# Performance work log

Hardware: AMD Instinct MI355X
Metric: run time of the kernel (lower is better)

## Reference

```python
import jax, jax.numpy as jnp
import numpy as np

B, T = 512, 64
A, H, R = 6, 256, 256
SS, SD = 32, 32          # stochastic_size, stochastic_dim
L = SS * SD              # latent_dim = 1024


def setup_inputs() -> dict:
    key = jax.random.key(0)
    ks = jax.random.split(key, 12)
    s = 0.05
    obs = jax.random.normal(ks[0], (B, T, H), dtype=jnp.float32)
    action = jax.random.normal(ks[1], (B, T, A), dtype=jnp.float32)
    first = jax.random.bernoulli(ks[2], 0.1, (B, T, 1))
    u = jax.random.uniform(ks[3], (T, B, SS, SD), minval=1e-6, maxval=1.0 - 1e-6)
    gumbel = -jnp.log(-jnp.log(u))  # Gumbel(0,1) noise for categorical sampling
    W_in = jax.random.normal(ks[4], (H, L + A)) * s
    b_in = jax.random.normal(ks[5], (H,)) * s
    W_ih = jax.random.normal(ks[6], (3 * R, H)) * s
    W_hh = jax.random.normal(ks[7], (3 * R, R)) * s
    b_ih = jax.random.normal(ks[8], (3 * R,)) * s
    b_hh = jax.random.normal(ks[9], (3 * R,)) * s
    W_post = jax.random.normal(ks[10], (L, R + H)) * s
    b_post = jax.random.normal(ks[11], (L,)) * s
    return {"obs": obs, "action": action, "first": first, "gumbel": gumbel,
            "W_in": W_in, "b_in": b_in, "W_ih": W_ih, "W_hh": W_hh,
            "b_ih": b_ih, "b_hh": b_hh, "W_post": W_post, "b_post": b_post}


def reference(obs, action, first, gumbel, W_in, b_in, W_ih, W_hh, b_ih, b_hh, W_post, b_post):
    bs = obs.shape[0]
    rec = W_hh.shape[1]
    latent = W_post.shape[0]
    size, dim = gumbel.shape[-2], gumbel.shape[-1]

    def step(carry, xs):
        deter, stoch = carry
        o, a, f, g = xs  # per-timestep slices
        # reset to initial (zeros) where episode starts
        deter = jnp.where(f, 0.0, deter)
        stoch = jnp.where(f, 0.0, stoch)
        # img_step: in-linear + GRUCell (torch gate order r, z, n)
        x = jnp.concatenate([stoch, a], axis=-1) @ W_in.T + b_in
        gi = x @ W_ih.T + b_ih
        gh = deter @ W_hh.T + b_hh
        i_r, i_z, i_n = jnp.split(gi, 3, axis=-1)
        h_r, h_z, h_n = jnp.split(gh, 3, axis=-1)
        r = jax.nn.sigmoid(i_r + h_r)
        z = jax.nn.sigmoid(i_z + h_z)
        n = jnp.tanh(i_n + r * h_n)
        h = (1.0 - z) * n + z * deter  # new deter
        # posterior head + categorical sample (Gumbel-max, non-differentiable)
        logits = jnp.concatenate([h, o], axis=-1) @ W_post.T + b_post
        lg = logits.reshape(bs, size, dim)
        idx = jnp.argmax(lg + g, axis=-1)
        stoch_new = jax.nn.one_hot(idx, dim, dtype=logits.dtype).reshape(bs, latent)
        return (h, stoch_new), (h, stoch_new, logits)

    carry0 = (jnp.zeros((bs, rec), obs.dtype), jnp.zeros((bs, latent), obs.dtype))
    xs = (jnp.swapaxes(obs, 0, 1), jnp.swapaxes(action, 0, 1),
          jnp.swapaxes(first, 0, 1), gumbel)
    _, (deter_seq, stoch_seq, logits_seq) = jax.lax.scan(step, carry0, xs)
    # back to batch-first [B, T, ...]
    return (jnp.swapaxes(deter_seq, 0, 1),
            jnp.swapaxes(stoch_seq, 0, 1),
            jnp.swapaxes(logits_seq, 0, 1))
```

## Files before the change

### kernel.cpp

```cpp
#include <hip/hip_runtime.h>
#include <math.h>

#define BB   512
#define TT   64
#define AD   6
#define HD   256
#define RD   256
#define LD   1024
#define GD   768
#define NB   2

#define OFF_WIHT    0u
#define OFF_WHHT    196608u
#define OFF_WPOSTT  393216u
#define OFF_WCT     917504u
#define OFF_BC      1708544u
#define OFF_OBSPROJ 1709312u
#define WS_FLOATS_FULL (OFF_OBSPROJ + (size_t)32768 * 1024)

__device__ __forceinline__ void fma4(float4& a, const float4 w, const float s) {
  a.x = fmaf(w.x, s, a.x); a.y = fmaf(w.y, s, a.y);
  a.z = fmaf(w.z, s, a.z); a.w = fmaf(w.w, s, a.w);
}
__device__ __forceinline__ void fma2(float2& a, const float2 w, const float s) {
  a.x = fmaf(w.x, s, a.x); a.y = fmaf(w.y, s, a.y);
}
typedef float fvec4 __attribute__((ext_vector_type(4)));
__device__ __forceinline__ float4 ntload4(const float* p) {
  const fvec4 v = __builtin_nontemporal_load((const fvec4*)p);
  return make_float4(v.x, v.y, v.z, v.w);
}
__device__ __forceinline__ void ntstore4(float* p, const float4 v) {
  fvec4 w; w.x = v.x; w.y = v.y; w.z = v.z; w.w = v.w;
  __builtin_nontemporal_store(w, (fvec4*)p);
}

__global__ __launch_bounds__(256) void transpose_k(const float* __restrict__ src,
                                                   float* __restrict__ dst,
                                                   int R, int C) {
  __shared__ float t_s[32][33];
  const int tx = threadIdx.x, ty = threadIdx.y;
  const int c0 = blockIdx.x * 32, r0 = blockIdx.y * 32;
#pragma unroll
  for (int k = 0; k < 4; ++k)
    t_s[ty + k*8][tx] = src[(size_t)(r0 + ty + k*8) * C + c0 + tx];
  __syncthreads();
#pragma unroll
  for (int k = 0; k < 4; ++k)
    dst[(size_t)(c0 + ty + k*8) * R + r0 + tx] = t_s[tx][ty + k*8];
}

__global__ __launch_bounds__(256) void wc_kernel(const float* __restrict__ W_in,
                                                 const float* __restrict__ b_in,
                                                 const float* __restrict__ WihT,
                                                 const float* __restrict__ b_ih,
                                                 float* __restrict__ WcT,
                                                 float* __restrict__ bc) {
  __shared__ float v_s[256];
  const int tid = threadIdx.x;
  const int col = blockIdx.x;
  v_s[tid] = (col < 1030) ? W_in[(size_t)tid * 1030 + col] : b_in[tid];
  __syncthreads();
  float a0 = 0.f, a1 = 0.f, a2 = 0.f;
#pragma unroll 4
  for (int h = 0; h < 256; ++h) {
    const float v = v_s[h];
    const float* row = &WihT[(size_t)h * GD];
    a0 = fmaf(row[tid      ], v, a0);
    a1 = fmaf(row[tid + 256], v, a1);
    a2 = fmaf(row[tid + 512], v, a2);
  }
  if (col < 1030) {
    WcT[(size_t)col * GD + tid      ] = a0;
    WcT[(size_t)col * GD + tid + 256] = a1;
    WcT[(size_t)col * GD + tid + 512] = a2;
  } else {
    bc[tid      ] = b_ih[tid      ] + a0;
    bc[tid + 256] = b_ih[tid + 256] + a1;
    bc[tid + 512] = b_ih[tid + 512] + a2;
  }
}

__global__ __launch_bounds__(256) void obsproj_gemm(const float* __restrict__ obs,
                                                    const float* __restrict__ Wpost,
                                                    const float* __restrict__ bpost,
                                                    float* __restrict__ outp) {
  __shared__ __align__(16) float As[32][132];
  __shared__ __align__(16) float Bs[32][132];
  const int tid = threadIdx.x;
  const int tx = tid & 15, ty = tid >> 4;
  const int m0 = blockIdx.y * 128, n0 = blockIdx.x * 128;
  float acc[8][8];
#pragma unroll
  for (int i = 0; i < 8; ++i)
#pragma unroll
    for (int j = 0; j < 8; ++j) acc[i][j] = 0.f;

  for (int k0 = 0; k0 < 256; k0 += 32) {
#pragma unroll
    for (int it = 0; it < 4; ++it) {
      const int idx = tid + it * 256;
      const int mi = idx >> 3, k4 = (idx & 7) * 4;
      float4 va = *(const float4*)&obs[(size_t)(m0 + mi) * 256 + k0 + k4];
      As[k4+0][mi] = va.x; As[k4+1][mi] = va.y; As[k4+2][mi] = va.z; As[k4+3][mi] = va.w;
      float4 vb = *(const float4*)&Wpost[(size_t)(n0 + mi) * 512 + 256 + k0 + k4];
      Bs[k4+0][mi] = vb.x; Bs[k4+1][mi] = vb.y; Bs[k4+2][mi] = vb.z; Bs[k4+3][mi] = vb.w;
    }
    __syncthreads();
#pragma unroll 8
    for (int k = 0; k < 32; ++k) {
      float4 a0 = *(const float4*)&As[k][ty*4];
      float4 a1 = *(const float4*)&As[k][64 + ty*4];
      float4 b0 = *(const float4*)&Bs[k][tx*4];
      float4 b1 = *(const float4*)&Bs[k][64 + tx*4];
      float av[8] = {a0.x,a0.y,a0.z,a0.w,a1.x,a1.y,a1.z,a1.w};
      float bv[8] = {b0.x,b0.y,b0.z,b0.w,b1.x,b1.y,b1.z,b1.w};
#pragma unroll
      for (int i = 0; i < 8; ++i)
#pragma unroll
        for (int j = 0; j < 8; ++j) acc[i][j] = fmaf(av[i], bv[j], acc[i][j]);
    }
    __syncthreads();
  }
  float4 bp0 = *(const float4*)&bpost[n0 + tx*4];
  float4 bp1 = *(const float4*)&bpost[n0 + 64 + tx*4];
#pragma unroll
  for (int i = 0; i < 8; ++i) {
    const int mi = (i < 4) ? (ty*4 + i) : (64 + ty*4 + (i - 4));
    float4 c0, c1;
    c0.x = acc[i][0] + bp0.x; c0.y = acc[i][1] + bp0.y;
    c0.z = acc[i][2] + bp0.z; c0.w = acc[i][3] + bp0.w;
    c1.x = acc[i][4] + bp1.x; c1.y = acc[i][5] + bp1.y;
    c1.z = acc[i][6] + bp1.z; c1.w = acc[i][7] + bp1.w;
    ntstore4(&outp[(size_t)(m0 + mi) * 1024 + n0 + tx*4], c0);
    ntstore4(&outp[(size_t)(m0 + mi) * 1024 + n0 + 64 + tx*4], c1);
  }
}

#define GH_LOAD(W, g) {                                                   \
    const int cg_ = (g) * 4;                                              \
    W[0] = wp[(size_t)(cg_ + 0) * 192];                                   \
    W[1] = wp[(size_t)(cg_ + 1) * 192];                                   \
    W[2] = wp[(size_t)(cg_ + 2) * 192];                                   \
    W[3] = wp[(size_t)(cg_ + 3) * 192];                                   \
  }
#define GH_LOADL(W) {                                                     \
    W[0] = ((const float4*)wpin_gh[half][0])[rg];                         \
    W[1] = ((const float4*)wpin_gh[half][1])[rg];                         \
    W[2] = ((const float4*)wpin_gh[half][2])[rg];                         \
    W[3] = ((const float4*)wpin_gh[half][3])[rg];                         \
  }
#define GH_FMA(W, g) {                                                    \
    const int cg_ = (g) * 4;                                              \
    const float4 d0 = *(const float4*)&deter_s[0][cbase + cg_];           \
    const float4 d1 = *(const float4*)&deter_s[1][cbase + cg_];           \
    fma4(acc0, W[0], d0.x); fma4(acc0, W[1], d0.y); fma4(acc0, W[2], d0.z); fma4(acc0, W[3], d0.w); \
    fma4(acc1, W[0], d1.x); fma4(acc1, W[1], d1.y); fma4(acc1, W[2], d1.z); fma4(acc1, W[3], d1.w); \
  }
#define GI_LOAD(W, g) {                                                   \
    W[0] = ntload4((const float*)&Wc4[(size_t)scol_s[j][(g)*4 + 0] * 192 + rg]); \
    W[1] = ntload4((const float*)&Wc4[(size_t)scol_s[j][(g)*4 + 1] * 192 + rg]); \
    W[2] = ntload4((const float*)&Wc4[(size_t)scol_s[j][(g)*4 + 2] * 192 + rg]); \
    W[3] = ntload4((const float*)&Wc4[(size_t)scol_s[j][(g)*4 + 3] * 192 + rg]); \
  }
#define GI_ADD(W) {                                                       \
    acc.x += W[0].x; acc.y += W[0].y; acc.z += W[0].z; acc.w += W[0].w;   \
    acc.x += W[1].x; acc.y += W[1].y; acc.z += W[1].z; acc.w += W[1].w;   \
    acc.x += W[2].x; acc.y += W[2].y; acc.z += W[2].z; acc.w += W[2].w;   \
    acc.x += W[3].x; acc.y += W[3].y; acc.z += W[3].z; acc.w += W[3].w;   \
  }
#define PP_LOAD(W, g) {                                                   \
    const int cg_ = (g) * 4;                                              \
    W[0] = pp2w[(size_t)(cg_ + 0) * 512];                                 \
    W[1] = pp2w[(size_t)(cg_ + 1) * 512];                                 \
    W[2] = pp2w[(size_t)(cg_ + 2) * 512];                                 \
    W[3] = pp2w[(size_t)(cg_ + 3) * 512];                                 \
  }
#define PP_LOADL(W, g) {                                                  \
    W[0] = ((const float2*)wpin_pp[half][g][0])[o2];                      \
    W[1] = ((const float2*)wpin_pp[half][g][1])[o2];                      \
    W[2] = ((const float2*)wpin_pp[half][g][2])[o2];                      \
    W[3] = ((const float2*)wpin_pp[half][g][3])[o2];                      \
  }
#define PP_FMA(W, g) {                                                    \
    const int cg_ = (g) * 4;                                              \
    const float4 d0 = *(const float4*)&deter_s[0][cbase + cg_];           \
    const float4 d1 = *(const float4*)&deter_s[1][cbase + cg_];           \
    fma2(acc0, W[0], d0.x); fma2(acc0, W[1], d0.y); fma2(acc0, W[2], d0.z); fma2(acc0, W[3], d0.w); \
    fma2(acc1, W[0], d1.x); fma2(acc1, W[1], d1.y); fma2(acc1, W[2], d1.z); fma2(acc1, W[3], d1.w); \
  }

__global__ __launch_bounds__(1024, 4) void rssm_scan(
    const float* __restrict__ obs, const float* __restrict__ action,
    const int* __restrict__ first, const float* __restrict__ gumbel,
    const float* __restrict__ WhhT, const float* __restrict__ WpostT,
    const float* __restrict__ WcT, const float* __restrict__ bc,
    const float* __restrict__ bhh, const float* __restrict__ bpost,
    const float* __restrict__ obsproj,
    float* __restrict__ out_deter, float* __restrict__ out_stoch,
    float* __restrict__ out_logits) {
  union SharedU {
    struct { float gi[NB][GD]; float ghp[2][NB][GD]; } g;
    float pp[2][NB][LD];
  };
  __shared__ SharedU u;
  __shared__ __align__(16) float deter_s[NB][RD];
  __shared__ __align__(16) float obs_s[NB][HD];
  __shared__ float act_all[NB][TT][AD];
  __shared__ int   first_all[NB][TT];
  __shared__ float bc_s[GD];
  __shared__ float bhh_s[GD];
  __shared__ int   scol_s[NB][32];
  __shared__ __align__(16) float wpin_gh[2][4][768];
  __shared__ __align__(16) float wpin_pp[2][2][4][1024];

  const int tid = threadIdx.x;
  const int b0 = blockIdx.x * NB;
  const bool use_op = (obsproj != nullptr);
  const float4* Wc4 = (const float4*)WcT;
  const float4* Wh4 = (const float4*)WhhT;
  const float2* Wp2 = (const float2*)WpostT;

  if (tid < NB * RD) deter_s[tid >> 8][tid & 255] = 0.f;
  if (tid < NB * TT * AD) {
    const int j = tid / (TT * AD), rem = tid % (TT * AD);
    act_all[j][rem / AD][rem % AD] = action[(size_t)(b0 + j) * TT * AD + rem];
  }
  if (tid < NB * TT) first_all[tid >> 6][tid & 63] = first[(b0 + (tid >> 6)) * TT + (tid & 63)];
  if (tid < GD) { bc_s[tid] = bc[tid]; bhh_s[tid] = bhh[tid]; }
  for (int i = tid; i < 1536; i += 1024) {
    const int hf = i / 768, r = i % 768, c = r / 192, rg = r % 192;
    ((float4*)wpin_gh[hf][c])[rg] = Wh4[(size_t)(hf * 128 + c) * 192 + rg];
  }
  for (int i = tid; i < 4096; i += 1024) {
    const int hf = i / 2048, r = i % 2048, g = r / 1024, r2 = r % 1024;
    const int c = r2 / 256, q = r2 % 256;
    ((float4*)wpin_pp[hf][g][c])[q] =
        ((const float4*)(WpostT + (size_t)(hf * 128 + g * 4 + c) * 1024))[q];
  }
  __syncthreads();

  const int jme = tid >> 8, o4me = tid & 255;

  for (int t = 0; t < TT; ++t) {
    float4 op4, g4;
    if (tid < NB * 256) {
      if (use_op)
        op4 = ntload4(&obsproj[(((size_t)(b0 + jme) * TT + t) * LD) + o4me * 4]);
      else
        op4 = *(const float4*)&bpost[o4me * 4];
      g4 = ntload4(&gumbel[(((size_t)t * BB + b0 + jme) * LD) + o4me * 4]);
    }

    if (tid < 384) {
      const int half = (tid < 192) ? 0 : 1;
      const int rg = tid - half * 192;
      const int cbase = half * 128;
      float4 acc0, acc1;
      if (half == 0) {
        acc0 = *(const float4*)&bhh_s[rg * 4];
        acc1 = acc0;
      } else {
        acc0 = make_float4(0.f, 0.f, 0.f, 0.f);
        acc1 = acc0;
      }
      const float4* wp = &Wh4[(size_t)cbase * 192 + rg];
      float4 wA[4], wB[4], wC[4];
      GH_LOAD(wA, 1); GH_LOAD(wB, 2);
      GH_LOADL(wC); GH_FMA(wC, 0);
#pragma unroll 1
      for (int gg = 0; gg < 9; ++gg) {
        const int g = 1 + gg * 3;
        GH_LOAD(wC, g + 2); GH_FMA(wA, g);
        GH_LOAD(wA, g + 3); GH_FMA(wB, g + 1);
        GH_LOAD(wB, g + 4); GH_FMA(wC, g + 2);
      }
      GH_LOAD(wC, 30); GH_FMA(wA, 28);
      GH_LOAD(wA, 31); GH_FMA(wB, 29);
      GH_FMA(wC, 30); GH_FMA(wA, 31);
      *(float4*)&u.g.ghp[half][0][rg * 4] = acc0;
      *(float4*)&u.g.ghp[half][1][rg * 4] = acc1;
    } else if (tid < 768) {
      const int task = tid - 384;
      const int j = task / 192, rg = task % 192;
      float4 acc = *(const float4*)&bc_s[rg * 4];
#pragma unroll
      for (int a = 0; a < AD; ++a)
        fma4(acc, Wc4[(size_t)(LD + a) * 192 + rg], act_all[j][t][a]);
      const bool skip = (t == 0) || first_all[j][t];
      if (!skip) {
        float4 gA[4], gB[4], gC[4];
        GI_LOAD(gA, 0); GI_LOAD(gB, 1);
#pragma unroll 1
        for (int gg = 0; gg < 2; ++gg) {
          const int g = gg * 3;
          GI_LOAD(gC, g + 2); GI_ADD(gA);
          GI_LOAD(gA, g + 3); GI_ADD(gB);
          GI_LOAD(gB, g + 4); GI_ADD(gC);
        }
        GI_ADD(gA); GI_ADD(gB);
      }
      *(float4*)&u.g.gi[j][rg * 4] = acc;
    } else {
      if (!use_op) {
        const int z = tid - 768;
        if (z < NB * 64) {
          const int j = z >> 6, r4 = z & 63;
          *(float4*)&obs_s[j][r4 * 4] =
              ntload4(&obs[((size_t)(b0 + j) * TT + t) * HD + r4 * 4]);
        }
      }
    }
    __syncthreads();

    if (tid < NB * RD) {
      const int j = tid >> 8, r = tid & 255;
      const float ir = u.g.gi[j][r], iz = u.g.gi[j][r + 256], inn = u.g.gi[j][r + 512];
      const float hr = u.g.ghp[0][j][r      ] + u.g.ghp[1][j][r      ];
      const float hz = u.g.ghp[0][j][r + 256] + u.g.ghp[1][j][r + 256];
      const float hn = u.g.ghp[0][j][r + 512] + u.g.ghp[1][j][r + 512];
      const bool f = (first_all[j][t] != 0);
      const float dprev = f ? 0.f : deter_s[j][r];
      const float rr = 1.f / (1.f + __expf(-(ir + hr)));
      const float zz = 1.f / (1.f + __expf(-(iz + hz)));
      const float nn = tanhf(fmaf(rr, hn, inn));
      const float h = (1.f - zz) * nn + zz * dprev;
      deter_s[j][r] = h;
      __builtin_nontemporal_store(h, &out_deter[((size_t)(b0 + j) * TT + t) * RD + r]);
    }
    __syncthreads();

    {
      const int half = tid >> 9, o2 = tid & 511;
      const int cbase = half * 128;
      float2 acc0 = make_float2(0.f, 0.f), acc1 = acc0;
      const float2* pp2w = &Wp2[(size_t)cbase * 512 + o2];
      float2 pA[4], pB[4], pC[4];
      PP_LOAD(pA, 2); PP_LOAD(pB, 3);
      PP_LOADL(pC, 0); PP_FMA(pC, 0);
      PP_LOADL(pC, 1); PP_FMA(pC, 1);
#pragma unroll 1
      for (int gg = 0; gg < 9; ++gg) {
        const int g = 2 + gg * 3;
        PP_LOAD(pC, g + 2); PP_FMA(pA, g);
        PP_LOAD(pA, g + 3); PP_FMA(pB, g + 1);
        PP_LOAD(pB, g + 4); PP_FMA(pC, g + 2);
      }
      PP_LOAD(pC, 31); PP_FMA(pA, 29);
      PP_FMA(pB, 30); PP_FMA(pC, 31);
      if (!use_op) {
#pragma unroll 4
        for (int c = 0; c < 128; c += 4) {
          const float2 w0 = Wp2[(size_t)(256 + cbase + c + 0) * 512 + o2];
          const float2 w1 = Wp2[(size_t)(256 + cbase + c + 1) * 512 + o2];
          const float2 w2 = Wp2[(size_t)(256 + cbase + c + 2) * 512 + o2];
          const float2 w3 = Wp2[(size_t)(256 + cbase + c + 3) * 512 + o2];
          const float4 o0 = *(const float4*)&obs_s[0][cbase + c];
          const float4 o1 = *(const float4*)&obs_s[1][cbase + c];
          fma2(acc0, w0, o0.x); fma2(acc0, w1, o0.y); fma2(acc0, w2, o0.z); fma2(acc0, w3, o0.w);
          fma2(acc1, w0, o1.x); fma2(acc1, w1, o1.y); fma2(acc1, w2, o1.z); fma2(acc1, w3, o1.w);
        }
      }
      *(float2*)&u.pp[half][0][o2 * 2] = acc0;
      *(float2*)&u.pp[half][1][o2 * 2] = acc1;
    }
    __syncthreads();

    {
      if (tid < NB * 256) {
        const float4 p0 = *(const float4*)&u.pp[0][jme][o4me * 4];
        const float4 p1 = *(const float4*)&u.pp[1][jme][o4me * 4];
        float4 l;
        l.x = p0.x + p1.x + op4.x; l.y = p0.y + p1.y + op4.y;
        l.z = p0.z + p1.z + op4.z; l.w = p0.w + p1.w + op4.w;
        ntstore4(&out_logits[((size_t)(b0 + jme) * TT + t) * LD + o4me * 4], l);
        float v[4] = {l.x + g4.x, l.y + g4.y, l.z + g4.z, l.w + g4.w};
        const int l0 = o4me * 4;
        float mv = v[0]; int mi = l0;
#pragma unroll
        for (int i = 1; i < 4; ++i)
          if (v[i] > mv) { mv = v[i]; mi = l0 + i; }
#pragma unroll
        for (int off = 1; off < 8; off <<= 1) {
          const float ov = __shfl_xor(mv, off);
          const int   oi = __shfl_xor(mi, off);
          if (ov > mv || (ov == mv && oi < mi)) { mv = ov; mi = oi; }
        }
        if ((o4me & 7) == 0) scol_s[jme][o4me >> 3] = mi;
        float4 oh;
        oh.x = (mi == l0 + 0) ? 1.f : 0.f;
        oh.y = (mi == l0 + 1) ? 1.f : 0.f;
        oh.z = (mi == l0 + 2) ? 1.f : 0.f;
        oh.w = (mi == l0 + 3) ? 1.f : 0.f;
        ntstore4(&out_stoch[((size_t)(b0 + jme) * TT + t) * LD + l0], oh);
      }
      if (tid < NB * 64) {
        const int j2 = tid >> 6, r4 = tid & 63;
        if (t + 1 < TT && first_all[j2][t + 1])
          *(float4*)&deter_s[j2][r4 * 4] = make_float4(0.f, 0.f, 0.f, 0.f);
      }
    }
    __syncthreads();
  }
}

extern "C" void kernel_launch(void* const* d_in, const int* in_sizes, int n_in,
                              void* d_out, int out_size, void* d_ws, size_t ws_size,
                              hipStream_t stream) {
  const float* obs    = (const float*)d_in[0];
  const float* action = (const float*)d_in[1];
  const int*   first  = (const int*)d_in[2];
  const float* gumbel = (const float*)d_in[3];
  const float* W_in   = (const float*)d_in[4];
  const float* b_in   = (const float*)d_in[5];
  const float* W_ih   = (const float*)d_in[6];
  const float* W_hh   = (const float*)d_in[7];
  const float* b_ih   = (const float*)d_in[8];
  const float* b_hh   = (const float*)d_in[9];
  const float* W_post = (const float*)d_in[10];
  const float* b_post = (const float*)d_in[11];

  float* ws      = (float*)d_ws;
  float* WihT    = ws + OFF_WIHT;
  float* WhhT    = ws + OFF_WHHT;
  float* WpostT  = ws + OFF_WPOSTT;
  float* WcT     = ws + OFF_WCT;
  float* bc      = ws + OFF_BC;
  float* obsproj = ws + OFF_OBSPROJ;
  const bool use_op = ws_size >= WS_FLOATS_FULL * sizeof(float);

  float* out_deter  = (float*)d_out;
  float* out_stoch  = out_deter + (size_t)BB * TT * RD;
  float* out_logits = out_stoch + (size_t)BB * TT * LD;

  transpose_k<<<dim3(256/32, 768/32), dim3(32, 8), 0, stream>>>(W_ih, WihT, 768, 256);
  transpose_k<<<dim3(256/32, 768/32), dim3(32, 8), 0, stream>>>(W_hh, WhhT, 768, 256);
  transpose_k<<<dim3(512/32, 1024/32), dim3(32, 8), 0, stream>>>(W_post, WpostT, 1024, 512);
  wc_kernel<<<1031, 256, 0, stream>>>(W_in, b_in, WihT, b_ih, WcT, bc);
  if (use_op)
    obsproj_gemm<<<dim3(1024/128, 32768/128), 256, 0, stream>>>(obs, W_post, b_post, obsproj);
  rssm_scan<<<BB/NB, 1024, 0, stream>>>(obs, action, first, gumbel, WhhT, WpostT, WcT, bc,
                                        b_hh, b_post, use_op ? obsproj : (const float*)nullptr,
                                        out_deter, out_stoch, out_logits);
}
```

Before: 2.597 ms.

## Process one batch row per block instead of two, doubling grid size

Each block of the recurrent scan now handles a single sequence instead of two, so the grid grows from 256 to 512 blocks and the launch-bounds occupancy hint is raised. The shared-memory pinned copy of the first W_post rows is removed, the projection loop restarts from row zero, and Wc gather loads lose their nontemporal hint. The aim is more parallel blocks and less shared memory per block, which may let more blocks fit on each CU. The cost is that each weight load from global memory now feeds only one sequence, which roughly doubles total weight traffic.

```diff
diff --git a/kernel.cpp b/kernel.cpp
--- a/kernel.cpp
+++ b/kernel.cpp
@@ -8,7 +8,6 @@
 #define RD   256
 #define LD   1024
 #define GD   768
-#define NB   2
 
 #define OFF_WIHT    0u
 #define OFF_WHHT    196608u
@@ -152,16 +151,14 @@
   }
 #define GH_FMA(W, g) {                                                    \
     const int cg_ = (g) * 4;                                              \
-    const float4 d0 = *(const float4*)&deter_s[0][cbase + cg_];           \
-    const float4 d1 = *(const float4*)&deter_s[1][cbase + cg_];           \
+    const float4 d0 = *(const float4*)&deter_s[cbase + cg_];              \
     fma4(acc0, W[0], d0.x); fma4(acc0, W[1], d0.y); fma4(acc0, W[2], d0.z); fma4(acc0, W[3], d0.w); \
-    fma4(acc1, W[0], d1.x); fma4(acc1, W[1], d1.y); fma4(acc1, W[2], d1.z); fma4(acc1, W[3], d1.w); \
   }
 #define GI_LOAD(W, g) {                                                   \
-    W[0] = ntload4((const float*)&Wc4[(size_t)scol_s[j][(g)*4 + 0] * 192 + rg]); \
-    W[1] = ntload4((const float*)&Wc4[(size_t)scol_s[j][(g)*4 + 1] * 192 + rg]); \
-    W[2] = ntload4((const float*)&Wc4[(size_t)scol_s[j][(g)*4 + 2] * 192 + rg]); \
-    W[3] = ntload4((const float*)&Wc4[(size_t)scol_s[j][(g)*4 + 3] * 192 + rg]); \
+    W[0] = Wc4[(size_t)scol_s[(g)*4 + 0] * 192 + rg];                     \
+    W[1] = Wc4[(size_t)scol_s[(g)*4 + 1] * 192 + rg];                     \
+    W[2] = Wc4[(size_t)scol_s[(g)*4 + 2] * 192 + rg];                     \
+    W[3] = Wc4[(size_t)scol_s[(g)*4 + 3] * 192 + rg];                     \
   }
 #define GI_ADD(W) {                                                       \
     acc.x += W[0].x; acc.y += W[0].y; acc.z += W[0].z; acc.w += W[0].w;   \
@@ -176,21 +173,13 @@
     W[2] = pp2w[(size_t)(cg_ + 2) * 512];                                 \
     W[3] = pp2w[(size_t)(cg_ + 3) * 512];                                 \
   }
-#define PP_LOADL(W, g) {                                                  \
-    W[0] = ((const float2*)wpin_pp[half][g][0])[o2];                      \
-    W[1] = ((const float2*)wpin_pp[half][g][1])[o2];                      \
-    W[2] = ((const float2*)wpin_pp[half][g][2])[o2];                      \
-    W[3] = ((const float2*)wpin_pp[half][g][3])[o2];                      \
-  }
 #define PP_FMA(W, g) {                                                    \
     const int cg_ = (g) * 4;                                              \
-    const float4 d0 = *(const float4*)&deter_s[0][cbase + cg_];           \
-    const float4 d1 = *(const float4*)&deter_s[1][cbase + cg_];           \
+    const float4 d0 = *(const float4*)&deter_s[cbase + cg_];              \
     fma2(acc0, W[0], d0.x); fma2(acc0, W[1], d0.y); fma2(acc0, W[2], d0.z); fma2(acc0, W[3], d0.w); \
-    fma2(acc1, W[0], d1.x); fma2(acc1, W[1], d1.y); fma2(acc1, W[2], d1.z); fma2(acc1, W[3], d1.w); \
-  }
-
-__global__ __launch_bounds__(1024, 4) void rssm_scan(
+  }
+
+__global__ __launch_bounds__(1024, 8) void rssm_scan(
     const float* __restrict__ obs, const float* __restrict__ action,
     const int* __restrict__ first, const float* __restrict__ gumbel,
     const float* __restrict__ WhhT, const float* __restrict__ WpostT,
@@ -200,70 +189,55 @@
     float* __restrict__ out_deter, float* __restrict__ out_stoch,
     float* __restrict__ out_logits) {
   union SharedU {
-    struct { float gi[NB][GD]; float ghp[2][NB][GD]; } g;
-    float pp[2][NB][LD];
+    struct { float gi[GD]; float ghp[2][GD]; } g;
+    float pp[2][LD];
   };
   __shared__ SharedU u;
-  __shared__ __align__(16) float deter_s[NB][RD];
-  __shared__ __align__(16) float obs_s[NB][HD];
-  __shared__ float act_all[NB][TT][AD];
-  __shared__ int   first_all[NB][TT];
+  __shared__ __align__(16) float deter_s[RD];
+  __shared__ __align__(16) float obs_s[HD];
+  __shared__ float act_all[TT][AD];
+  __shared__ int   first_all[TT];
   __shared__ float bc_s[GD];
   __shared__ float bhh_s[GD];
-  __shared__ int   scol_s[NB][32];
+  __shared__ int   scol_s[32];
   __shared__ __align__(16) float wpin_gh[2][4][768];
-  __shared__ __align__(16) float wpin_pp[2][2][4][1024];
 
   const int tid = threadIdx.x;
-  const int b0 = blockIdx.x * NB;
+  const int b0 = blockIdx.x;
   const bool use_op = (obsproj != nullptr);
   const float4* Wc4 = (const float4*)WcT;
   const float4* Wh4 = (const float4*)WhhT;
   const float2* Wp2 = (const float2*)WpostT;
 
-  if (tid < NB * RD) deter_s[tid >> 8][tid & 255] = 0.f;
-  if (tid < NB * TT * AD) {
-    const int j = tid / (TT * AD), rem = tid % (TT * AD);
-    act_all[j][rem / AD][rem % AD] = action[(size_t)(b0 + j) * TT * AD + rem];
-  }
-  if (tid < NB * TT) first_all[tid >> 6][tid & 63] = first[(b0 + (tid >> 6)) * TT + (tid & 63)];
+  if (tid < RD) deter_s[tid] = 0.f;
+  if (tid < TT * AD) act_all[tid / AD][tid % AD] = action[(size_t)b0 * TT * AD + tid];
+  if (tid < TT) first_all[tid] = first[b0 * TT + tid];
   if (tid < GD) { bc_s[tid] = bc[tid]; bhh_s[tid] = bhh[tid]; }
   for (int i = tid; i < 1536; i += 1024) {
     const int hf = i / 768, r = i % 768, c = r / 192, rg = r % 192;
     ((float4*)wpin_gh[hf][c])[rg] = Wh4[(size_t)(hf * 128 + c) * 192 + rg];
   }
-  for (int i = tid; i < 4096; i += 1024) {
-    const int hf = i / 2048, r = i % 2048, g = r / 1024, r2 = r % 1024;
-    const int c = r2 / 256, q = r2 % 256;
-    ((float4*)wpin_pp[hf][g][c])[q] =
-        ((const float4*)(WpostT + (size_t)(hf * 128 + g * 4 + c) * 1024))[q];
-  }
   __syncthreads();
 
-  const int jme = tid >> 8, o4me = tid & 255;
+  const int o4me = tid & 255;
 
   for (int t = 0; t < TT; ++t) {
     float4 op4, g4;
-    if (tid < NB * 256) {
+    if (tid < 256) {
       if (use_op)
-        op4 = ntload4(&obsproj[(((size_t)(b0 + jme) * TT + t) * LD) + o4me * 4]);
+        op4 = ntload4(&obsproj[(((size_t)b0 * TT + t) * LD) + o4me * 4]);
       else
         op4 = *(const float4*)&bpost[o4me * 4];
-      g4 = ntload4(&gumbel[(((size_t)t * BB + b0 + jme) * LD) + o4me * 4]);
+      g4 = ntload4(&gumbel[(((size_t)t * BB + b0) * LD) + o4me * 4]);
     }
 
     if (tid < 384) {
       const int half = (tid < 192) ? 0 : 1;
       const int rg = tid - half * 192;
       const int cbase = half * 128;
-      float4 acc0, acc1;
-      if (half == 0) {
-        acc0 = *(const float4*)&bhh_s[rg * 4];
-        acc1 = acc0;
-      } else {
-        acc0 = make_float4(0.f, 0.f, 0.f, 0.f);
-        acc1 = acc0;
-      }
+      float4 acc0;
+      if (half == 0) acc0 = *(const float4*)&bhh_s[rg * 4];
+      else           acc0 = make_float4(0.f, 0.f, 0.f, 0.f);
       const float4* wp = &Wh4[(size_t)cbase * 192 + rg];
       float4 wA[4], wB[4], wC[4];
       GH_LOAD(wA, 1); GH_LOAD(wB, 2);
@@ -278,16 +252,14 @@
       GH_LOAD(wC, 30); GH_FMA(wA, 28);
       GH_LOAD(wA, 31); GH_FMA(wB, 29);
       GH_FMA(wC, 30); GH_FMA(wA, 31);
-      *(float4*)&u.g.ghp[half][0][rg * 4] = acc0;
-      *(float4*)&u.g.ghp[half][1][rg * 4] = acc1;
-    } else if (tid < 768) {
-      const int task = tid - 384;
-      const int j = task / 192, rg = task % 192;
+      *(float4*)&u.g.ghp[half][rg * 4] = acc0;
+    } else if (tid < 576) {
+      const int rg = tid - 384;
       float4 acc = *(const float4*)&bc_s[rg * 4];
 #pragma unroll
       for (int a = 0; a < AD; ++a)
-        fma4(acc, Wc4[(size_t)(LD + a) * 192 + rg], act_all[j][t][a]);
-      const bool skip = (t == 0) || first_all[j][t];
+        fma4(acc, Wc4[(size_t)(LD + a) * 192 + rg], act_all[t][a]);
+      const bool skip = (t == 0) || first_all[t];
       if (!skip) {
         float4 gA[4], gB[4], gC[4];
         GI_LOAD(gA, 0); GI_LOAD(gB, 1);
@@ -300,54 +272,50 @@
         }
         GI_ADD(gA); GI_ADD(gB);
       }
-      *(float4*)&u.g.gi[j][rg * 4] = acc;
+      *(float4*)&u.g.gi[rg * 4] = acc;
     } else {
       if (!use_op) {
-        const int z = tid - 768;
-        if (z < NB * 64) {
-          const int j = z >> 6, r4 = z & 63;
-          *(float4*)&obs_s[j][r4 * 4] =
-              ntload4(&obs[((size_t)(b0 + j) * TT + t) * HD + r4 * 4]);
+        const int z = tid - 576;
+        if (z < 64) {
+          *(float4*)&obs_s[z * 4] =
+              ntload4(&obs[((size_t)b0 * TT + t) * HD + z * 4]);
         }
       }
     }
     __syncthreads();
 
-    if (tid < NB * RD) {
-      const int j = tid >> 8, r = tid & 255;
-      const float ir = u.g.gi[j][r], iz = u.g.gi[j][r + 256], inn = u.g.gi[j][r + 512];
-      const float hr = u.g.ghp[0][j][r      ] + u.g.ghp[1][j][r      ];
-      const float hz = u.g.ghp[0][j][r + 256] + u.g.ghp[1][j][r + 256];
-      const float hn = u.g.ghp[0][j][r + 512] + u.g.ghp[1][j][r + 512];
-      const bool f = (first_all[j][t] != 0);
-      const float dprev = f ? 0.f : deter_s[j][r];
+    if (tid < RD) {
+      const int r = tid;
+      const float ir = u.g.gi[r], iz = u.g.gi[r + 256], inn = u.g.gi[r + 512];
+      const float hr = u.g.ghp[0][r      ] + u.g.ghp[1][r      ];
+      const float hz = u.g.ghp[0][r + 256] + u.g.ghp[1][r + 256];
+      const float hn = u.g.ghp[0][r + 512] + u.g.ghp[1][r + 512];
+      const bool f = (first_all[t] != 0);
+      const float dprev = f ? 0.f : deter_s[r];
       const float rr = 1.f / (1.f + __expf(-(ir + hr)));
       const float zz = 1.f / (1.f + __expf(-(iz + hz)));
       const float nn = tanhf(fmaf(rr, hn, inn));
       const float h = (1.f - zz) * nn + zz * dprev;
-      deter_s[j][r] = h;
-      __builtin_nontemporal_store(h, &out_deter[((size_t)(b0 + j) * TT + t) * RD + r]);
+      deter_s[r] = h;
+      __builtin_nontemporal_store(h, &out_deter[((size_t)b0 * TT + t) * RD + r]);
     }
     __syncthreads();
 
     {
       const int half = tid >> 9, o2 = tid & 511;
       const int cbase = half * 128;
-      float2 acc0 = make_float2(0.f, 0.f), acc1 = acc0;
+      float2 acc0 = make_float2(0.f, 0.f);
       const float2* pp2w = &Wp2[(size_t)cbase * 512 + o2];
       float2 pA[4], pB[4], pC[4];
-      PP_LOAD(pA, 2); PP_LOAD(pB, 3);
-      PP_LOADL(pC, 0); PP_FMA(pC, 0);
-      PP_LOADL(pC, 1); PP_FMA(pC, 1);
+      PP_LOAD(pA, 0); PP_LOAD(pB, 1);
 #pragma unroll 1
-      for (int gg = 0; gg < 9; ++gg) {
-        const int g = 2 + gg * 3;
+      for (int gg = 0; gg < 10; ++gg) {
+        const int g = gg * 3;
         PP_LOAD(pC, g + 2); PP_FMA(pA, g);
         PP_LOAD(pA, g + 3); PP_FMA(pB, g + 1);
         PP_LOAD(pB, g + 4); PP_FMA(pC, g + 2);
       }
-      PP_LOAD(pC, 31); PP_FMA(pA, 29);
-      PP_FMA(pB, 30); PP_FMA(pC, 31);
+      PP_FMA(pA, 30); PP_FMA(pB, 31);
       if (!use_op) {
 #pragma unroll 4
         for (int c = 0; c < 128; c += 4) {
@@ -355,25 +323,22 @@
           const float2 w1 = Wp2[(size_t)(256 + cbase + c + 1) * 512 + o2];
           const float2 w2 = Wp2[(size_t)(256 + cbase + c + 2) * 512 + o2];
           const float2 w3 = Wp2[(size_t)(256 + cbase + c + 3) * 512 + o2];
-          const float4 o0 = *(const float4*)&obs_s[0][cbase + c];
-          const float4 o1 = *(const float4*)&obs_s[1][cbase + c];
+          const float4 o0 = *(const float4*)&obs_s[cbase + c];
           fma2(acc0, w0, o0.x); fma2(acc0, w1, o0.y); fma2(acc0, w2, o0.z); fma2(acc0, w3, o0.w);
-          fma2(acc1, w0, o1.x); fma2(acc1, w1, o1.y); fma2(acc1, w2, o1.z); fma2(acc1, w3, o1.w);
         }
       }
-      *(float2*)&u.pp[half][0][o2 * 2] = acc0;
-      *(float2*)&u.pp[half][1][o2 * 2] = acc1;
+      *(float2*)&u.pp[half][o2 * 2] = acc0;
     }
     __syncthreads();
 
     {
-      if (tid < NB * 256) {
-        const float4 p0 = *(const float4*)&u.pp[0][jme][o4me * 4];
-        const float4 p1 = *(const float4*)&u.pp[1][jme][o4me * 4];
+      if (tid < 256) {
+        const float4 p0 = *(const float4*)&u.pp[0][o4me * 4];
+        const float4 p1 = *(const float4*)&u.pp[1][o4me * 4];
         float4 l;
         l.x = p0.x + p1.x + op4.x; l.y = p0.y + p1.y + op4.y;
         l.z = p0.z + p1.z + op4.z; l.w = p0.w + p1.w + op4.w;
-        ntstore4(&out_logits[((size_t)(b0 + jme) * TT + t) * LD + o4me * 4], l);
+        ntstore4(&out_logits[((size_t)b0 * TT + t) * LD + o4me * 4], l);
         float v[4] = {l.x + g4.x, l.y + g4.y, l.z + g4.z, l.w + g4.w};
         const int l0 = o4me * 4;
         float mv = v[0]; int mi = l0;
@@ -386,18 +351,17 @@
           const int   oi = __shfl_xor(mi, off);
           if (ov > mv || (ov == mv && oi < mi)) { mv = ov; mi = oi; }
         }
-        if ((o4me & 7) == 0) scol_s[jme][o4me >> 3] = mi;
+        if ((o4me & 7) == 0) scol_s[o4me >> 3] = mi;
         float4 oh;
         oh.x = (mi == l0 + 0) ? 1.f : 0.f;
         oh.y = (mi == l0 + 1) ? 1.f : 0.f;
         oh.z = (mi == l0 + 2) ? 1.f : 0.f;
         oh.w = (mi == l0 + 3) ? 1.f : 0.f;
-        ntstore4(&out_stoch[((size_t)(b0 + jme) * TT + t) * LD + l0], oh);
-      }
-      if (tid < NB * 64) {
-        const int j2 = tid >> 6, r4 = tid & 63;
-        if (t + 1 < TT && first_all[j2][t + 1])
-          *(float4*)&deter_s[j2][r4 * 4] = make_float4(0.f, 0.f, 0.f, 0.f);
+        ntstore4(&out_stoch[((size_t)b0 * TT + t) * LD + l0], oh);
+      }
+      if (tid < 64) {
+        if (t + 1 < TT && first_all[t + 1])
+          *(float4*)&deter_s[tid * 4] = make_float4(0.f, 0.f, 0.f, 0.f);
       }
     }
     __syncthreads();
@@ -439,7 +403,7 @@
   wc_kernel<<<1031, 256, 0, stream>>>(W_in, b_in, WihT, b_ih, WcT, bc);
   if (use_op)
     obsproj_gemm<<<dim3(1024/128, 32768/128), 256, 0, stream>>>(obs, W_post, b_post, obsproj);
-  rssm_scan<<<BB/NB, 1024, 0, stream>>>(obs, action, first, gumbel, WhhT, WpostT, WcT, bc,
-                                        b_hh, b_post, use_op ? obsproj : (const float*)nullptr,
-                                        out_deter, out_stoch, out_logits);
-}
+  rssm_scan<<<BB, 1024, 0, stream>>>(obs, action, first, gumbel, WhhT, WpostT, WcT, bc,
+                                     b_hh, b_post, use_op ? obsproj : (const float*)nullptr,
+                                     out_deter, out_stoch, out_logits);
+}
```

Measured after the change: 3.989 ms. 1.54x slower.
